# Performance work log

Hardware: AMD Instinct MI355X
Metric: run time of the kernel (lower is better)

## Reference

```python
import jax, jax.numpy as jnp
import numpy as np

N = 100000   # nodes
E = 1600000  # edges (avg degree 16)
N_IN, N_HID, N_OUT = 64, 64, 16


def setup_inputs() -> dict:
    key = jax.random.key(0)
    k1, k2, k3, k4 = jax.random.split(key, 4)
    x = jax.random.normal(k1, (N, N_IN), dtype=jnp.float32)
    edge_index = jax.random.randint(k2, (2, E), 0, N, dtype=jnp.int64)
    # Glorot-style init like PyG GCNConv linear weights
    W1 = jax.random.normal(k3, (N_IN, N_HID), dtype=jnp.float32) * (1.0 / np.sqrt(N_IN))
    b1 = jnp.zeros((N_HID,), dtype=jnp.float32)
    W2 = jax.random.normal(k4, (N_HID, N_OUT), dtype=jnp.float32) * (1.0 / np.sqrt(N_HID))
    b2 = jnp.zeros((N_OUT,), dtype=jnp.float32)
    return {"x": x, "edge_index": edge_index, "W1": W1, "b1": b1, "W2": W2, "b2": b2}


def reference(x, edge_index, W1, b1, W2, b2):
    n = x.shape[0]
    # GCNConv default: add self-loops with weight 1, symmetric normalization
    loop = jnp.arange(n, dtype=edge_index.dtype)
    src = jnp.concatenate([edge_index[0], loop])  # [E+N]
    dst = jnp.concatenate([edge_index[1], loop])  # [E+N]
    w = jnp.ones(src.shape[0], dtype=x.dtype)
    deg = jax.ops.segment_sum(w, dst, num_segments=n)           # in-degree incl. self-loop
    dinv = jnp.where(deg > 0, jax.lax.rsqrt(deg), 0.0)
    norm = dinv[src] * w * dinv[dst]                            # [E+N] edge coefficients

    def gcn_conv(h, Wm, bm):
        h = h @ Wm                                              # [N, d_out] linear first (PyG order)
        msg = h[src] * norm[:, None]                            # gather + scale
        return jax.ops.segment_sum(msg, dst, num_segments=n) + bm  # scatter-add + bias

    h = jax.nn.relu(gcn_conv(x, W1, b1))
    # dropout is identity at inference (training=False)
    return jax.nn.log_softmax(gcn_conv(h, W2, b2), axis=1)
```

## Files before the change

### kernel.cpp

```cpp
#include <hip/hip_runtime.h>

constexpr int FIN = 64;
constexpr int FH  = 64;
constexpr int FO  = 16;


constexpr int BSH      = 7;
constexpr int BW       = 1 << BSH;
constexpr int NBUCK    = 1024;
constexpr int EPB_HIST = 16384;
constexpr int EPB_BIN  = 4096;

__device__ inline unsigned short f2bf(float f) {
    unsigned u = __float_as_uint(f);
    return (unsigned short)((u + 0x7FFFu + ((u >> 16) & 1u)) >> 16);
}
__device__ inline float bf2f(unsigned short h) {
    return __uint_as_float((unsigned)h << 16);
}
__device__ inline float4 bf4_to_f4(ushort4 u) {
    float4 f;
    f.x = bf2f(u.x); f.y = bf2f(u.y); f.z = bf2f(u.z); f.w = bf2f(u.w);
    return f;
}

__launch_bounds__(256)
__global__ void hist_kernel(const int* __restrict__ ei, int E, int* __restrict__ bcnt) {
    __shared__ int lh[NBUCK];
    int t = threadIdx.x;
    for (int i = t; i < NBUCK; i += 256) lh[i] = 0;
    __syncthreads();
    int base = blockIdx.x * EPB_HIST;
    int lim  = min(E, base + EPB_HIST);
    for (int e = base + t; e < lim; e += 256)
        atomicAdd(&lh[ei[E + e] >> BSH], 1);
    __syncthreads();
    for (int b = t; b < NBUCK; b += 256) {
        int c = lh[b];
        if (c > 0) atomicAdd(&bcnt[b], c);
    }
}

__launch_bounds__(1024)
__global__ void bucket_scan_kernel(const int* __restrict__ bcnt, int* __restrict__ bbase,
                                   int* __restrict__ gcur, int* __restrict__ offs,
                                   int N, int E) {
    __shared__ int s[NBUCK];
    int t = threadIdx.x;
    int v = bcnt[t];
    s[t] = v;
    __syncthreads();
    for (int d = 1; d < NBUCK; d <<= 1) {
        int u = (t >= d) ? s[t - d] : 0;
        __syncthreads();
        s[t] += u;
        __syncthreads();
    }
    int ex = s[t] - v;
    bbase[t] = ex;
    gcur[t]  = ex;
    if (t == NBUCK - 1) {
        bbase[NBUCK] = s[t];
        offs[N] = E;
    }
}

__device__ inline void binning_body(const int* __restrict__ ei, int E, int chunk,
                                    int* __restrict__ gcur, unsigned* __restrict__ ebuf,
                                    int* lh) {
    int t = threadIdx.x;
    for (int i = t; i < NBUCK; i += 256) lh[i] = 0;
    __syncthreads();
    int base = chunk * EPB_BIN;
    int lim  = min(E, base + EPB_BIN);
    for (int e = base + t; e < lim; e += 256)
        atomicAdd(&lh[ei[E + e] >> BSH], 1);
    __syncthreads();
    for (int b = t; b < NBUCK; b += 256) {
        int c = lh[b];
        lh[b] = (c > 0) ? atomicAdd(&gcur[b], c) : 0;
    }
    __syncthreads();
    for (int e = base + t; e < lim; e += 256) {
        int d = ei[E + e];
        int srcv = ei[e];
        int pos = atomicAdd(&lh[d >> BSH], 1);
        ebuf[pos] = (unsigned)srcv | ((unsigned)(d & (BW - 1)) << 17);
    }
}

__launch_bounds__(256)
__global__ void binning_kernel(const int* __restrict__ ei, int E,
                               int* __restrict__ gcur, unsigned* __restrict__ ebuf) {
    __shared__ int lh[NBUCK];
    binning_body(ei, E, blockIdx.x, gcur, ebuf, lh);
}

__launch_bounds__(256, 4)
__global__ void gemm1_binning_kernel(const float* __restrict__ x, const float* __restrict__ W1,
                                     unsigned short* __restrict__ hsb,
                                     const int* __restrict__ ei, int E,
                                     int* __restrict__ gcur, unsigned* __restrict__ ebuf,
                                     int N, int NBIN) {
    __shared__ float smem[FIN * FH];
    int tid = threadIdx.x;
    if ((int)blockIdx.x < NBIN) {
        binning_body(ei, E, (int)blockIdx.x, gcur, ebuf, (int*)smem);
        return;
    }
    float* Ws = smem;
    {
        const float4* W14 = (const float4*)W1;
        float4* Ws4 = (float4*)smem;
        for (int i = tid; i < 1024; i += 256) Ws4[i] = W14[i];
    }
    __syncthreads();
    int cg = tid & 15;
    int rg = tid >> 4;
    int rowBase = ((int)blockIdx.x - NBIN) * 64;
    int r0 = rowBase + rg * 4;
    const float4* x4 = (const float4*)x;
    size_t ra = (size_t)min(r0 + 0, N - 1) * 16;
    size_t rb = (size_t)min(r0 + 1, N - 1) * 16;
    size_t rc = (size_t)min(r0 + 2, N - 1) * 16;
    size_t rd = (size_t)min(r0 + 3, N - 1) * 16;
    float4 acc0 = {0,0,0,0}, acc1 = {0,0,0,0}, acc2 = {0,0,0,0}, acc3 = {0,0,0,0};
    #pragma unroll 2
    for (int kc = 0; kc < 16; ++kc) {
        float4 xa0 = x4[ra + kc];
        float4 xa1 = x4[rb + kc];
        float4 xa2 = x4[rc + kc];
        float4 xa3 = x4[rd + kc];
        const float* xa0f = (const float*)&xa0;
        const float* xa1f = (const float*)&xa1;
        const float* xa2f = (const float*)&xa2;
        const float* xa3f = (const float*)&xa3;
        #pragma unroll
        for (int j = 0; j < 4; ++j) {
            float4 wv = *(const float4*)&Ws[(kc * 4 + j) * FH + cg * 4];
            float v0 = xa0f[j], v1 = xa1f[j], v2 = xa2f[j], v3 = xa3f[j];
            acc0.x = fmaf(v0, wv.x, acc0.x); acc0.y = fmaf(v0, wv.y, acc0.y);
            acc0.z = fmaf(v0, wv.z, acc0.z); acc0.w = fmaf(v0, wv.w, acc0.w);
            acc1.x = fmaf(v1, wv.x, acc1.x); acc1.y = fmaf(v1, wv.y, acc1.y);
            acc1.z = fmaf(v1, wv.z, acc1.z); acc1.w = fmaf(v1, wv.w, acc1.w);
            acc2.x = fmaf(v2, wv.x, acc2.x); acc2.y = fmaf(v2, wv.y, acc2.y);
            acc2.z = fmaf(v2, wv.z, acc2.z); acc2.w = fmaf(v2, wv.w, acc2.w);
            acc3.x = fmaf(v3, wv.x, acc3.x); acc3.y = fmaf(v3, wv.y, acc3.y);
            acc3.z = fmaf(v3, wv.z, acc3.z); acc3.w = fmaf(v3, wv.w, acc3.w);
        }
    }
    ushort4* hsb4 = (ushort4*)hsb;
    if (r0 + 0 < N) hsb4[(size_t)(r0 + 0) * 16 + cg] =
        make_ushort4(f2bf(acc0.x), f2bf(acc0.y), f2bf(acc0.z), f2bf(acc0.w));
    if (r0 + 1 < N) hsb4[(size_t)(r0 + 1) * 16 + cg] =
        make_ushort4(f2bf(acc1.x), f2bf(acc1.y), f2bf(acc1.z), f2bf(acc1.w));
    if (r0 + 2 < N) hsb4[(size_t)(r0 + 2) * 16 + cg] =
        make_ushort4(f2bf(acc2.x), f2bf(acc2.y), f2bf(acc2.z), f2bf(acc2.w));
    if (r0 + 3 < N) hsb4[(size_t)(r0 + 3) * 16 + cg] =
        make_ushort4(f2bf(acc3.x), f2bf(acc3.y), f2bf(acc3.z), f2bf(acc3.w));
}

__launch_bounds__(256)
__global__ void bucket_csr_kernel(const unsigned* __restrict__ ebuf,
                                  const int* __restrict__ bbase,
                                  int* __restrict__ csr, int* __restrict__ offs,
                                  float* __restrict__ dinv, int N) {
    __shared__ int cnt[BW], sc[BW], cur[BW];
    int t = threadIdx.x;
    int b = blockIdx.x;
    if (t < BW) cnt[t] = 0;
    __syncthreads();
    int beg = bbase[b], end = bbase[b + 1];
    for (int i = beg + t; i < end; i += 256)
        atomicAdd(&cnt[ebuf[i] >> 17], 1);
    __syncthreads();
    if (t < BW) sc[t] = cnt[t];
    __syncthreads();
    for (int d = 1; d < BW; d <<= 1) {
        int u = (t < BW && t >= d) ? sc[t - d] : 0;
        __syncthreads();
        if (t < BW) sc[t] += u;
        __syncthreads();
    }
    int nodeBase = b << BSH;
    if (t < BW) {
        int node = nodeBase + t;
        int ex = beg + sc[t] - cnt[t];
        cur[t] = ex;
        if (node < N) {
            offs[node] = ex;
            dinv[node] = rsqrtf((float)(cnt[t] + 1));
        }
    }
    __syncthreads();
    for (int i = beg + t; i < end; i += 256) {
        unsigned w = ebuf[i];
        int pos = atomicAdd(&cur[w >> 17], 1);
        csr[pos] = (int)(w & 0x1FFFF);
    }
}

__launch_bounds__(256)
__global__ void agg1_gemm2_kernel(const unsigned short* __restrict__ hsb,
                                  const int* __restrict__ csr,
                                  const int* __restrict__ offs, const float* __restrict__ dinv,
                                  const float* __restrict__ b1, const float* __restrict__ W2,
                                  unsigned short* __restrict__ hs2b, int N) {
    __shared__ float W2s[FH * FO];
    __shared__ float h1s[16][68];
    const ushort4* hs4 = (const ushort4*)hsb;
    int tid = threadIdx.x;
    for (int i = tid; i < FH * FO; i += 256) W2s[i] = W2[i];
    int g = tid >> 4, l = tid & 15;
    int n = blockIdx.x * 16 + g;
    if (n < N) {
        float di_n = dinv[n];
        float4 self = bf4_to_f4(hs4[(size_t)n * 16 + l]);
        float4 acc;
        acc.x = self.x * di_n; acc.y = self.y * di_n;
        acc.z = self.z * di_n; acc.w = self.w * di_n;
        int j = offs[n], end = offs[n + 1];
        for (; j + 7 < end; j += 8) {
            int s0 = csr[j],     s1 = csr[j + 1], s2 = csr[j + 2], s3 = csr[j + 3];
            int s4 = csr[j + 4], s5 = csr[j + 5], s6 = csr[j + 6], s7 = csr[j + 7];
            float d0 = dinv[s0], d1 = dinv[s1], d2 = dinv[s2], d3 = dinv[s3];
            float d4 = dinv[s4], d5 = dinv[s5], d6 = dinv[s6], d7 = dinv[s7];
            float4 a0 = bf4_to_f4(hs4[(size_t)s0 * 16 + l]);
            float4 a1 = bf4_to_f4(hs4[(size_t)s1 * 16 + l]);
            float4 a2 = bf4_to_f4(hs4[(size_t)s2 * 16 + l]);
            float4 a3 = bf4_to_f4(hs4[(size_t)s3 * 16 + l]);
            float4 a4 = bf4_to_f4(hs4[(size_t)s4 * 16 + l]);
            float4 a5 = bf4_to_f4(hs4[(size_t)s5 * 16 + l]);
            float4 a6 = bf4_to_f4(hs4[(size_t)s6 * 16 + l]);
            float4 a7 = bf4_to_f4(hs4[(size_t)s7 * 16 + l]);
            acc.x += (fmaf(a0.x, d0, a1.x * d1) + fmaf(a2.x, d2, a3.x * d3))
                   + (fmaf(a4.x, d4, a5.x * d5) + fmaf(a6.x, d6, a7.x * d7));
            acc.y += (fmaf(a0.y, d0, a1.y * d1) + fmaf(a2.y, d2, a3.y * d3))
                   + (fmaf(a4.y, d4, a5.y * d5) + fmaf(a6.y, d6, a7.y * d7));
            acc.z += (fmaf(a0.z, d0, a1.z * d1) + fmaf(a2.z, d2, a3.z * d3))
                   + (fmaf(a4.z, d4, a5.z * d5) + fmaf(a6.z, d6, a7.z * d7));
            acc.w += (fmaf(a0.w, d0, a1.w * d1) + fmaf(a2.w, d2, a3.w * d3))
                   + (fmaf(a4.w, d4, a5.w * d5) + fmaf(a6.w, d6, a7.w * d7));
        }
        for (; j + 1 < end; j += 2) {
            int s0 = csr[j], s1 = csr[j + 1];
            float d0 = dinv[s0], d1 = dinv[s1];
            float4 a0 = bf4_to_f4(hs4[(size_t)s0 * 16 + l]);
            float4 a1 = bf4_to_f4(hs4[(size_t)s1 * 16 + l]);
            acc.x += fmaf(a0.x, d0, a1.x * d1);
            acc.y += fmaf(a0.y, d0, a1.y * d1);
            acc.z += fmaf(a0.z, d0, a1.z * d1);
            acc.w += fmaf(a0.w, d0, a1.w * d1);
        }
        if (j < end) {
            int s0 = csr[j];
            float d0 = dinv[s0];
            float4 a0 = bf4_to_f4(hs4[(size_t)s0 * 16 + l]);
            acc.x = fmaf(a0.x, d0, acc.x); acc.y = fmaf(a0.y, d0, acc.y);
            acc.z = fmaf(a0.z, d0, acc.z); acc.w = fmaf(a0.w, d0, acc.w);
        }
        float4 bb = ((const float4*)b1)[l];
        float4 h;
        h.x = fmaxf(fmaf(di_n, acc.x, bb.x), 0.f);
        h.y = fmaxf(fmaf(di_n, acc.y, bb.y), 0.f);
        h.z = fmaxf(fmaf(di_n, acc.z, bb.z), 0.f);
        h.w = fmaxf(fmaf(di_n, acc.w, bb.w), 0.f);
        *((float4*)&h1s[g][l * 4]) = h;
    }
    __syncthreads();
    int r = tid >> 4, o = tid & 15;
    int n2 = blockIdx.x * 16 + r;
    if (n2 < N) {
        float acc = 0.f;
        #pragma unroll
        for (int jj = 0; jj < FH; ++jj)
            acc = fmaf(h1s[r][jj], W2s[jj * FO + o], acc);
        hs2b[(size_t)n2 * FO + o] = f2bf(acc * dinv[n2]);
    }
}

__launch_bounds__(256)
__global__ void agg2_softmax_kernel(const unsigned short* __restrict__ hs2b,
                                    const int* __restrict__ csr,
                                    const int* __restrict__ offs, const float* __restrict__ dinv,
                                    const float* __restrict__ b2, float* __restrict__ out, int N) {
    int tid = threadIdx.x;
    int g = tid >> 4, o = tid & 15;
    int n = blockIdx.x * 16 + g;
    float v = 0.f;
    if (n < N) {
        float acc = bf2f(hs2b[(size_t)n * 16 + o]);
        int j = offs[n], end = offs[n + 1];
        for (; j + 7 < end; j += 8) {
            int s0 = csr[j],     s1 = csr[j + 1], s2 = csr[j + 2], s3 = csr[j + 3];
            int s4 = csr[j + 4], s5 = csr[j + 5], s6 = csr[j + 6], s7 = csr[j + 7];
            float t0 = bf2f(hs2b[(size_t)s0 * 16 + o]) + bf2f(hs2b[(size_t)s1 * 16 + o]);
            float t1 = bf2f(hs2b[(size_t)s2 * 16 + o]) + bf2f(hs2b[(size_t)s3 * 16 + o]);
            float t2 = bf2f(hs2b[(size_t)s4 * 16 + o]) + bf2f(hs2b[(size_t)s5 * 16 + o]);
            float t3 = bf2f(hs2b[(size_t)s6 * 16 + o]) + bf2f(hs2b[(size_t)s7 * 16 + o]);
            acc += (t0 + t1) + (t2 + t3);
        }
        for (; j < end; ++j) acc += bf2f(hs2b[(size_t)csr[j] * 16 + o]);
        v = fmaf(dinv[n], acc, b2[o]);
    }
    float m = v;
    #pragma unroll
    for (int s = 8; s >= 1; s >>= 1) m = fmaxf(m, __shfl_xor(m, s, 64));
    float ex = __expf(v - m);
    float sum = ex;
    #pragma unroll
    for (int s = 8; s >= 1; s >>= 1) sum += __shfl_xor(sum, s, 64);
    if (n < N) out[(size_t)n * FO + o] = v - m - __logf(sum);
}

extern "C" void kernel_launch(void* const* d_in, const int* in_sizes, int n_in,
                              void* d_out, int out_size, void* d_ws, size_t ws_size,
                              hipStream_t stream) {
    const float* x  = (const float*)d_in[0];
    const int*   ei = (const int*)d_in[1];
    const float* W1 = (const float*)d_in[2];
    const float* b1 = (const float*)d_in[3];
    const float* W2 = (const float*)d_in[4];
    const float* b2 = (const float*)d_in[5];
    float* out = (float*)d_out;

    const int N = in_sizes[0] / FIN;
    const int E = in_sizes[1] / 2;
    const int NCH  = (E + EPB_HIST - 1) / EPB_HIST;
    const int NCB  = (E + EPB_BIN - 1) / EPB_BIN;
    const int NB4  = (N + BW - 1) / BW;
    const int G1T  = (N + 63) / 64;
    const int GA   = (N + 15) / 16;

    char* ws = (char*)d_ws;
    size_t off = 0;
    auto alloc = [&](size_t bytes) -> void* {
        off = (off + 255) & ~(size_t)255;
        void* p = ws + off;
        off += bytes;
        return p;
    };
    float*          dinv  = (float*)alloc((size_t)N * 4);
    unsigned short* hsb   = (unsigned short*)alloc((size_t)N * FH * 2);
    unsigned short* hs2b  = (unsigned short*)alloc((size_t)N * FO * 2);
    int*            offs  = (int*)alloc((size_t)(N + 1) * 4);
    int*            bcnt  = (int*)alloc(NBUCK * 4);
    int*            bbase = (int*)alloc((NBUCK + 1) * 4);
    int*            gcur  = (int*)alloc(NBUCK * 4);
    unsigned* ebuf;
    int*      csr;
    bool ws_fits = (ws_size >= off + 512 + (size_t)E * 8);
    if (ws_fits) {
        ebuf = (unsigned*)alloc((size_t)E * 4);
        csr  = (int*)     alloc((size_t)E * 4);
    } else {
        ebuf = (unsigned*)x;
        csr  = (int*)x + E;
    }

    hipMemsetAsync(bcnt, 0, NBUCK * 4, stream);

    hist_kernel<<<NCH, 256, 0, stream>>>(ei, E, bcnt);
    bucket_scan_kernel<<<1, NBUCK, 0, stream>>>(bcnt, bbase, gcur, offs, N, E);
    if (ws_fits) {
        gemm1_binning_kernel<<<NCB + G1T, 256, 0, stream>>>(x, W1, hsb, ei, E,
                                                            gcur, ebuf, N, NCB);
    } else {
        gemm1_binning_kernel<<<G1T, 256, 0, stream>>>(x, W1, hsb, ei, E,
                                                      gcur, ebuf, N, 0);
        binning_kernel<<<NCB, 256, 0, stream>>>(ei, E, gcur, ebuf);
    }
    bucket_csr_kernel<<<NB4, 256, 0, stream>>>(ebuf, bbase, csr, offs, dinv, N);
    agg1_gemm2_kernel<<<GA, 256, 0, stream>>>(hsb, csr, offs, dinv, b1, W2, hs2b, N);
    agg2_softmax_kernel<<<GA, 256, 0, stream>>>(hs2b, csr, offs, dinv, b2, out, N);
}
```

Before: 213.2 us.

## Precompute per-chunk bucket offsets and prescale layer-1 features by source dinv

```diff
diff --git a/kernel.cpp b/kernel.cpp
--- a/kernel.cpp
+++ b/kernel.cpp
@@ -5,11 +5,10 @@
 constexpr int FO  = 16;
 
 
-constexpr int BSH      = 7;
-constexpr int BW       = 1 << BSH;
-constexpr int NBUCK    = 1024;
-constexpr int EPB_HIST = 16384;
-constexpr int EPB_BIN  = 4096;
+constexpr int BSH   = 7;
+constexpr int BW    = 1 << BSH;
+constexpr int NBUCK = 1024;
+constexpr int EPB   = 4096;
 
 __device__ inline unsigned short f2bf(float f) {
     unsigned u = __float_as_uint(f);
@@ -25,26 +24,28 @@
 }
 
 __launch_bounds__(256)
-__global__ void hist_kernel(const int* __restrict__ ei, int E, int* __restrict__ bcnt) {
+__global__ void hist_kernel(const int* __restrict__ ei, int E,
+                            int* __restrict__ ccnt, int* __restrict__ bcnt) {
     __shared__ int lh[NBUCK];
     int t = threadIdx.x;
     for (int i = t; i < NBUCK; i += 256) lh[i] = 0;
     __syncthreads();
-    int base = blockIdx.x * EPB_HIST;
-    int lim  = min(E, base + EPB_HIST);
+    int base = blockIdx.x * EPB;
+    int lim  = min(E, base + EPB);
     for (int e = base + t; e < lim; e += 256)
         atomicAdd(&lh[ei[E + e] >> BSH], 1);
     __syncthreads();
+    int* crow = ccnt + (size_t)blockIdx.x * NBUCK;
     for (int b = t; b < NBUCK; b += 256) {
         int c = lh[b];
+        crow[b] = c;
         if (c > 0) atomicAdd(&bcnt[b], c);
     }
 }
 
 __launch_bounds__(1024)
 __global__ void bucket_scan_kernel(const int* __restrict__ bcnt, int* __restrict__ bbase,
-                                   int* __restrict__ gcur, int* __restrict__ offs,
-                                   int N, int E) {
+                                   int* __restrict__ offs, int N, int E) {
     __shared__ int s[NBUCK];
     int t = threadIdx.x;
     int v = bcnt[t];
@@ -56,31 +57,56 @@
         s[t] += u;
         __syncthreads();
     }
-    int ex = s[t] - v;
-    bbase[t] = ex;
-    gcur[t]  = ex;
+    bbase[t] = s[t] - v;
     if (t == NBUCK - 1) {
         bbase[NBUCK] = s[t];
         offs[N] = E;
     }
 }
 
+__launch_bounds__(256)
+__global__ void chunk_scan_kernel(int* __restrict__ ccnt, const int* __restrict__ bbase,
+                                  int nchunk) {
+    int b = blockIdx.x * 256 + threadIdx.x;
+    if (b >= NBUCK) return;
+    int base = bbase[b];
+    int c = 0;
+    for (; c + 8 <= nchunk; c += 8) {
+        int* p0 = &ccnt[(size_t)(c + 0) * NBUCK + b];
+        int* p1 = &ccnt[(size_t)(c + 1) * NBUCK + b];
+        int* p2 = &ccnt[(size_t)(c + 2) * NBUCK + b];
+        int* p3 = &ccnt[(size_t)(c + 3) * NBUCK + b];
+        int* p4 = &ccnt[(size_t)(c + 4) * NBUCK + b];
+        int* p5 = &ccnt[(size_t)(c + 5) * NBUCK + b];
+        int* p6 = &ccnt[(size_t)(c + 6) * NBUCK + b];
+        int* p7 = &ccnt[(size_t)(c + 7) * NBUCK + b];
+        int v0 = *p0, v1 = *p1, v2 = *p2, v3 = *p3;
+        int v4 = *p4, v5 = *p5, v6 = *p6, v7 = *p7;
+        *p0 = base; base += v0;
+        *p1 = base; base += v1;
+        *p2 = base; base += v2;
+        *p3 = base; base += v3;
+        *p4 = base; base += v4;
+        *p5 = base; base += v5;
+        *p6 = base; base += v6;
+        *p7 = base; base += v7;
+    }
+    for (; c < nchunk; ++c) {
+        int* p = &ccnt[(size_t)c * NBUCK + b];
+        int v = *p;
+        *p = base; base += v;
+    }
+}
+
 __device__ inline void binning_body(const int* __restrict__ ei, int E, int chunk,
-                                    int* __restrict__ gcur, unsigned* __restrict__ ebuf,
-                                    int* lh) {
+                                    const int* __restrict__ cbase,
+                                    unsigned* __restrict__ ebuf, int* lh) {
     int t = threadIdx.x;
-    for (int i = t; i < NBUCK; i += 256) lh[i] = 0;
-    __syncthreads();
-    int base = chunk * EPB_BIN;
-    int lim  = min(E, base + EPB_BIN);
-    for (int e = base + t; e < lim; e += 256)
-        atomicAdd(&lh[ei[E + e] >> BSH], 1);
-    __syncthreads();
-    for (int b = t; b < NBUCK; b += 256) {
-        int c = lh[b];
-        lh[b] = (c > 0) ? atomicAdd(&gcur[b], c) : 0;
-    }
-    __syncthreads();
+    const int* crow = cbase + (size_t)chunk * NBUCK;
+    for (int i = t; i < NBUCK; i += 256) lh[i] = crow[i];
+    __syncthreads();
+    int base = chunk * EPB;
+    int lim  = min(E, base + EPB);
     for (int e = base + t; e < lim; e += 256) {
         int d = ei[E + e];
         int srcv = ei[e];
@@ -91,21 +117,21 @@
 
 __launch_bounds__(256)
 __global__ void binning_kernel(const int* __restrict__ ei, int E,
-                               int* __restrict__ gcur, unsigned* __restrict__ ebuf) {
+                               const int* __restrict__ cbase, unsigned* __restrict__ ebuf) {
     __shared__ int lh[NBUCK];
-    binning_body(ei, E, blockIdx.x, gcur, ebuf, lh);
+    binning_body(ei, E, blockIdx.x, cbase, ebuf, lh);
 }
 
 __launch_bounds__(256, 4)
 __global__ void gemm1_binning_kernel(const float* __restrict__ x, const float* __restrict__ W1,
                                      unsigned short* __restrict__ hsb,
                                      const int* __restrict__ ei, int E,
-                                     int* __restrict__ gcur, unsigned* __restrict__ ebuf,
+                                     const int* __restrict__ cbase, unsigned* __restrict__ ebuf,
                                      int N, int NBIN) {
     __shared__ float smem[FIN * FH];
     int tid = threadIdx.x;
     if ((int)blockIdx.x < NBIN) {
-        binning_body(ei, E, (int)blockIdx.x, gcur, ebuf, (int*)smem);
+        binning_body(ei, E, (int)blockIdx.x, cbase, ebuf, (int*)smem);
         return;
     }
     float* Ws = smem;
@@ -164,8 +190,10 @@
 __global__ void bucket_csr_kernel(const unsigned* __restrict__ ebuf,
                                   const int* __restrict__ bbase,
                                   int* __restrict__ csr, int* __restrict__ offs,
-                                  float* __restrict__ dinv, int N) {
+                                  float* __restrict__ dinv, unsigned short* __restrict__ hsb,
+                                  int N) {
     __shared__ int cnt[BW], sc[BW], cur[BW];
+    __shared__ float dval[BW];
     int t = threadIdx.x;
     int b = blockIdx.x;
     if (t < BW) cnt[t] = 0;
@@ -187,9 +215,11 @@
         int node = nodeBase + t;
         int ex = beg + sc[t] - cnt[t];
         cur[t] = ex;
+        float di = rsqrtf((float)(cnt[t] + 1));
+        dval[t] = di;
         if (node < N) {
             offs[node] = ex;
-            dinv[node] = rsqrtf((float)(cnt[t] + 1));
+            dinv[node] = di;
         }
     }
     __syncthreads();
@@ -197,6 +227,16 @@
         unsigned w = ebuf[i];
         int pos = atomicAdd(&cur[w >> 17], 1);
         csr[pos] = (int)(w & 0x1FFFF);
+    }
+    int nNodes = min(BW, N - nodeBase);
+    ushort4* h4 = (ushort4*)hsb;
+    for (int k = t; k < nNodes * 16; k += 256) {
+        int ln = k >> 4, c = k & 15;
+        float di = dval[ln];
+        size_t idx = (size_t)(nodeBase + ln) * 16 + c;
+        float4 f = bf4_to_f4(h4[idx]);
+        h4[idx] = make_ushort4(f2bf(f.x * di), f2bf(f.y * di),
+                               f2bf(f.z * di), f2bf(f.w * di));
     }
 }
 
@@ -215,16 +255,11 @@
     int n = blockIdx.x * 16 + g;
     if (n < N) {
         float di_n = dinv[n];
-        float4 self = bf4_to_f4(hs4[(size_t)n * 16 + l]);
-        float4 acc;
-        acc.x = self.x * di_n; acc.y = self.y * di_n;
-        acc.z = self.z * di_n; acc.w = self.w * di_n;
+        float4 acc = bf4_to_f4(hs4[(size_t)n * 16 + l]);
         int j = offs[n], end = offs[n + 1];
         for (; j + 7 < end; j += 8) {
             int s0 = csr[j],     s1 = csr[j + 1], s2 = csr[j + 2], s3 = csr[j + 3];
             int s4 = csr[j + 4], s5 = csr[j + 5], s6 = csr[j + 6], s7 = csr[j + 7];
-            float d0 = dinv[s0], d1 = dinv[s1], d2 = dinv[s2], d3 = dinv[s3];
-            float d4 = dinv[s4], d5 = dinv[s5], d6 = dinv[s6], d7 = dinv[s7];
             float4 a0 = bf4_to_f4(hs4[(size_t)s0 * 16 + l]);
             float4 a1 = bf4_to_f4(hs4[(size_t)s1 * 16 + l]);
             float4 a2 = bf4_to_f4(hs4[(size_t)s2 * 16 + l]);
@@ -233,31 +268,21 @@
             float4 a5 = bf4_to_f4(hs4[(size_t)s5 * 16 + l]);
             float4 a6 = bf4_to_f4(hs4[(size_t)s6 * 16 + l]);
             float4 a7 = bf4_to_f4(hs4[(size_t)s7 * 16 + l]);
-            acc.x += (fmaf(a0.x, d0, a1.x * d1) + fmaf(a2.x, d2, a3.x * d3))
-                   + (fmaf(a4.x, d4, a5.x * d5) + fmaf(a6.x, d6, a7.x * d7));
-            acc.y += (fmaf(a0.y, d0, a1.y * d1) + fmaf(a2.y, d2, a3.y * d3))
-                   + (fmaf(a4.y, d4, a5.y * d5) + fmaf(a6.y, d6, a7.y * d7));
-            acc.z += (fmaf(a0.z, d0, a1.z * d1) + fmaf(a2.z, d2, a3.z * d3))
-                   + (fmaf(a4.z, d4, a5.z * d5) + fmaf(a6.z, d6, a7.z * d7));
-            acc.w += (fmaf(a0.w, d0, a1.w * d1) + fmaf(a2.w, d2, a3.w * d3))
-                   + (fmaf(a4.w, d4, a5.w * d5) + fmaf(a6.w, d6, a7.w * d7));
+            acc.x += ((a0.x + a1.x) + (a2.x + a3.x)) + ((a4.x + a5.x) + (a6.x + a7.x));
+            acc.y += ((a0.y + a1.y) + (a2.y + a3.y)) + ((a4.y + a5.y) + (a6.y + a7.y));
+            acc.z += ((a0.z + a1.z) + (a2.z + a3.z)) + ((a4.z + a5.z) + (a6.z + a7.z));
+            acc.w += ((a0.w + a1.w) + (a2.w + a3.w)) + ((a4.w + a5.w) + (a6.w + a7.w));
         }
         for (; j + 1 < end; j += 2) {
             int s0 = csr[j], s1 = csr[j + 1];
-            float d0 = dinv[s0], d1 = dinv[s1];
             float4 a0 = bf4_to_f4(hs4[(size_t)s0 * 16 + l]);
             float4 a1 = bf4_to_f4(hs4[(size_t)s1 * 16 + l]);
-            acc.x += fmaf(a0.x, d0, a1.x * d1);
-            acc.y += fmaf(a0.y, d0, a1.y * d1);
-            acc.z += fmaf(a0.z, d0, a1.z * d1);
-            acc.w += fmaf(a0.w, d0, a1.w * d1);
+            acc.x += a0.x + a1.x; acc.y += a0.y + a1.y;
+            acc.z += a0.z + a1.z; acc.w += a0.w + a1.w;
         }
         if (j < end) {
-            int s0 = csr[j];
-            float d0 = dinv[s0];
-            float4 a0 = bf4_to_f4(hs4[(size_t)s0 * 16 + l]);
-            acc.x = fmaf(a0.x, d0, acc.x); acc.y = fmaf(a0.y, d0, acc.y);
-            acc.z = fmaf(a0.z, d0, acc.z); acc.w = fmaf(a0.w, d0, acc.w);
+            float4 a0 = bf4_to_f4(hs4[(size_t)csr[j] * 16 + l]);
+            acc.x += a0.x; acc.y += a0.y; acc.z += a0.z; acc.w += a0.w;
         }
         float4 bb = ((const float4*)b1)[l];
         float4 h;
@@ -326,8 +351,7 @@
 
     const int N = in_sizes[0] / FIN;
     const int E = in_sizes[1] / 2;
-    const int NCH  = (E + EPB_HIST - 1) / EPB_HIST;
-    const int NCB  = (E + EPB_BIN - 1) / EPB_BIN;
+    const int NCB  = (E + EPB - 1) / EPB;
     const int NB4  = (N + BW - 1) / BW;
     const int G1T  = (N + 63) / 64;
     const int GA   = (N + 15) / 16;
@@ -346,7 +370,7 @@
     int*            offs  = (int*)alloc((size_t)(N + 1) * 4);
     int*            bcnt  = (int*)alloc(NBUCK * 4);
     int*            bbase = (int*)alloc((NBUCK + 1) * 4);
-    int*            gcur  = (int*)alloc(NBUCK * 4);
+    int*            ccnt  = (int*)alloc((size_t)NCB * NBUCK * 4);
     unsigned* ebuf;
     int*      csr;
     bool ws_fits = (ws_size >= off + 512 + (size_t)E * 8);
@@ -360,17 +384,18 @@
 
     hipMemsetAsync(bcnt, 0, NBUCK * 4, stream);
 
-    hist_kernel<<<NCH, 256, 0, stream>>>(ei, E, bcnt);
-    bucket_scan_kernel<<<1, NBUCK, 0, stream>>>(bcnt, bbase, gcur, offs, N, E);
+    hist_kernel<<<NCB, 256, 0, stream>>>(ei, E, ccnt, bcnt);
+    bucket_scan_kernel<<<1, NBUCK, 0, stream>>>(bcnt, bbase, offs, N, E);
+    chunk_scan_kernel<<<NBUCK / 256, 256, 0, stream>>>(ccnt, bbase, NCB);
     if (ws_fits) {
         gemm1_binning_kernel<<<NCB + G1T, 256, 0, stream>>>(x, W1, hsb, ei, E,
-                                                            gcur, ebuf, N, NCB);
+                                                            ccnt, ebuf, N, NCB);
     } else {
         gemm1_binning_kernel<<<G1T, 256, 0, stream>>>(x, W1, hsb, ei, E,
-                                                      gcur, ebuf, N, 0);
-        binning_kernel<<<NCB, 256, 0, stream>>>(ei, E, gcur, ebuf);
-    }
-    bucket_csr_kernel<<<NB4, 256, 0, stream>>>(ebuf, bbase, csr, offs, dinv, N);
+                                                      ccnt, ebuf, N, 0);
+        binning_kernel<<<NCB, 256, 0, stream>>>(ei, E, ccnt, ebuf);
+    }
+    bucket_csr_kernel<<<NB4, 256, 0, stream>>>(ebuf, bbase, csr, offs, dinv, hsb, N);
     agg1_gemm2_kernel<<<GA, 256, 0, stream>>>(hsb, csr, offs, dinv, b1, W2, hs2b, N);
     agg2_softmax_kernel<<<GA, 256, 0, stream>>>(hs2b, csr, offs, dinv, b2, out, N);
 }
```

New measurement: 228.2 us. +7.1%, slower.
